# Kernel optimization log

Measured on AMD Instinct MI355X. Metric: run time of the kernel, lower is better.

## Reference

```python
import jax, jax.numpy as jnp
import numpy as np

F, LP, NL, DG = 65536, 8, 8192, 64
D = 32  # path_state_dim == link_state_dim
ITERS = 8
MS = {'flow_traffic': (0.5, 2.0), 'flow_length': (0.5, 2.0), 'flow_loss_packet': (0.1, 5.0),
      'flow_propag_delay': (0.2, 3.0), 'link_capacity': (1.0, 1.0)}


def gru_cell(h, x, w, u, b):
    # Keras GRUCell (reset_after=True); gate order z, r, h
    mx = x @ w + b[0]
    mh = h @ u + b[1]
    xz, xr, xh = jnp.split(mx, 3, axis=-1)
    hz, hr, hh = jnp.split(mh, 3, axis=-1)
    z = jax.nn.sigmoid(xz + hz)
    r = jax.nn.sigmoid(xr + hr)
    c = jnp.tanh(xh + r * hh)
    return z * h + (1.0 - z) * c


def setup_inputs() -> dict:
    key = jax.random.key(0)
    ks = jax.random.split(key, 24)
    g = lambda i, shape: jax.random.normal(ks[i], shape, jnp.float32) * 0.1
    return dict(
        flow_traffic=jax.random.uniform(ks[0], (F, 1), jnp.float32),
        flow_length=jax.random.uniform(ks[1], (F, 1), jnp.float32),
        flow_loss_packet=jax.random.uniform(ks[2], (F, 1), jnp.float32),
        flow_propag_delay=jax.random.uniform(ks[3], (F, 1), jnp.float32),
        flow_packet_size=jax.random.uniform(ks[4], (F, 1), jnp.float32),
        link_capacity=jax.random.uniform(ks[5], (NL, 1), jnp.float32) + 0.5,
        link_to_flow=jax.random.randint(ks[6], (F, LP), 0, NL),
        flow_to_link_flow=jax.random.randint(ks[7], (NL, DG), 0, F),
        flow_to_link_pos=jax.random.randint(ks[8], (NL, DG), 0, LP + 1),
        fe_w1=g(9, (4, D)), fe_b1=jnp.zeros(D), fe_w2=g(10, (D, D)), fe_b2=jnp.zeros(D),
        le_w1=g(11, (2, D)), le_b1=jnp.zeros(D), le_w2=g(12, (D, D)), le_b2=jnp.zeros(D),
        att_w=g(13, (D, D)), att_b=jnp.zeros(D),
        pg_w=g(14, (D, 3 * D)), pg_u=g(15, (D, 3 * D)), pg_b=jnp.zeros((2, 3 * D)),
        lg_w=g(16, (D, 3 * D)), lg_u=g(17, (D, 3 * D)), lg_b=jnp.zeros((2, 3 * D)),
        ro_w1=g(18, (D, D // 2)), ro_b1=jnp.zeros(D // 2),
        ro_w2=g(19, (D // 2, D // 4)), ro_b2=jnp.zeros(D // 4),
        ro_w3=g(20, (D // 4, 1)), ro_b3=jnp.zeros(1),
    )


def reference(flow_traffic, flow_length, flow_loss_packet, flow_propag_delay, flow_packet_size,
              link_capacity, link_to_flow, flow_to_link_flow, flow_to_link_pos,
              fe_w1, fe_b1, fe_w2, fe_b2, le_w1, le_b1, le_w2, le_b2, att_w, att_b,
              pg_w, pg_u, pg_b, lg_w, lg_u, lg_b, ro_w1, ro_b1, ro_w2, ro_b2, ro_w3, ro_b3):
    norm = lambda x, k: (x - MS[k][0]) * MS[k][1]
    # per-link load: mean of traffic of flows crossing it / capacity  -> [NL,1]
    load = jnp.mean(flow_traffic[flow_to_link_flow], axis=1) / link_capacity
    pf = jnp.concatenate([norm(flow_traffic, 'flow_traffic'), norm(flow_length, 'flow_length'),
                          norm(flow_loss_packet, 'flow_loss_packet'),
                          norm(flow_propag_delay, 'flow_propag_delay')], axis=1)
    path_state = jax.nn.selu(jax.nn.selu(pf @ fe_w1 + fe_b1) @ fe_w2 + fe_b2)  # [F,D]
    lf = jnp.concatenate([norm(link_capacity, 'link_capacity'), load], axis=1)
    link_state = jax.nn.selu(jax.nn.selu(lf @ le_w1 + le_b1) @ le_w2 + le_b2)  # [NL,D]

    pss = None
    for _ in range(ITERS):
        link_gather = link_state[link_to_flow]  # [F,LP,D]
        prev = path_state

        def step(h, x):
            h2 = gru_cell(h, x, pg_w, pg_u, pg_b)
            return h2, h2

        path_state, seq = jax.lax.scan(step, prev, jnp.swapaxes(link_gather, 0, 1))
        seq = jnp.swapaxes(seq, 0, 1)  # [F,LP,D]
        pss = jnp.concatenate([prev[:, None, :], seq], axis=1)  # [F,LP+1,D]
        path_gather = pss[flow_to_link_flow, flow_to_link_pos]  # [NL,DG,D]
        attn = jax.nn.leaky_relu(path_gather @ att_w + att_b, negative_slope=0.2)
        score = jax.nn.softmax(attn, axis=-1)  # K.softmax default axis=-1
        agg = jnp.sum(score * path_gather, axis=1)  # [NL,D]
        link_state = gru_cell(link_state, agg, lg_w, lg_u, lg_b)

    h = jax.nn.selu(pss[:, 1:] @ ro_w1 + ro_b1)
    h = jax.nn.selu(h @ ro_w2 + ro_b2)
    occupancy = jax.nn.softplus(h @ ro_w3 + ro_b3)  # [F,LP,1]
    capacity_gather = link_capacity[link_to_flow]  # [F,LP,1]
    delay = jnp.sum(occupancy / capacity_gather, axis=1)  # [F,1]
    return delay + flow_propag_delay
```

## Files before the change

kernel.cpp:

```cpp
#include <hip/hip_runtime.h>
#include <hip/hip_bf16.h>
#include <cstddef>

#define F_    65536
#define LP_   8
#define NL_   8192
#define DG_   64
#define D_    32
#define ITERS_ 8

typedef short bf16x8 __attribute__((ext_vector_type(8)));
typedef float f32x2 __attribute__((ext_vector_type(2)));
typedef float f32x4 __attribute__((ext_vector_type(4)));
typedef float f32x16 __attribute__((ext_vector_type(16)));
typedef unsigned int u32x4 __attribute__((ext_vector_type(4)));

__device__ __forceinline__ float sigmoidf_(float x) { return 1.0f / (1.0f + __expf(-x)); }
__device__ __forceinline__ float tanhf_(float x)    { return 1.0f - 2.0f / (__expf(2.0f * x) + 1.0f); }
__device__ __forceinline__ float seluf_(float x) {
    const float a = 1.6732632423543772f, s = 1.0507009873554805f;
    return x > 0.0f ? s * x : s * a * (__expf(x) - 1.0f);
}
__device__ __forceinline__ float softplusf_(float x) { return x > 20.0f ? x : log1pf(__expf(x)); }

#define REP32(M) M(0)M(1)M(2)M(3)M(4)M(5)M(6)M(7)M(8)M(9)M(10)M(11)M(12)M(13)M(14)M(15) \
                 M(16)M(17)M(18)M(19)M(20)M(21)M(22)M(23)M(24)M(25)M(26)M(27)M(28)M(29)M(30)M(31)

#define BC32(src, i) __int_as_float(__builtin_amdgcn_ds_swizzle(__float_as_int(src), ((i) << 5)))

__device__ __forceinline__ unsigned int cvtpk_bf16(float a, float b) {
    unsigned int r;
    asm("v_cvt_pk_bf16_f32 %0, %1, %2" : "=v"(r) : "v"(a), "v"(b));
    return r;
}
__device__ __forceinline__ float bf_lo(unsigned int u) { return __uint_as_float(u << 16); }
__device__ __forceinline__ float bf_hi(unsigned int u) { return __uint_as_float(u & 0xFFFF0000u); }

__device__ __forceinline__ void mk_frag_w(f32x4 v0, f32x4 v1, u32x4& uh, u32x4& ul) {
    uh.x = cvtpk_bf16(v0.x, v0.y);
    uh.y = cvtpk_bf16(v0.z, v0.w);
    uh.z = cvtpk_bf16(v1.x, v1.y);
    uh.w = cvtpk_bf16(v1.z, v1.w);
    ul.x = cvtpk_bf16(v0.x - bf_lo(uh.x), v0.y - bf_hi(uh.x));
    ul.y = cvtpk_bf16(v0.z - bf_lo(uh.y), v0.w - bf_hi(uh.y));
    ul.z = cvtpk_bf16(v1.x - bf_lo(uh.z), v1.y - bf_hi(uh.z));
    ul.w = cvtpk_bf16(v1.z - bf_lo(uh.w), v1.w - bf_hi(uh.w));
}
__device__ __forceinline__ void mk_frag(f32x4 v0, f32x4 v1, bf16x8& hi, bf16x8& lo) {
    u32x4 uh, ul;
    mk_frag_w(v0, v1, uh, ul);
    hi = __builtin_bit_cast(bf16x8, uh);
    lo = __builtin_bit_cast(bf16x8, ul);
}

__device__ __forceinline__ int mxoff(int g, int d) { return g * 32 + (d & 15) * 2 + (d >> 4); }

__global__ __launch_bounds__(256) void k_init_path(
    const float* __restrict__ tr, const float* __restrict__ len,
    const float* __restrict__ loss, const float* __restrict__ prop,
    const float* __restrict__ fe_w1, const float* __restrict__ fe_b1,
    const float* __restrict__ fe_w2, const float* __restrict__ fe_b2,
    float* __restrict__ h32)
{
    const int j = threadIdx.x & 31;
    const int half = (threadIdx.x >> 5) & 1;
    float w2c[32];
#pragma unroll
    for (int i = 0; i < 32; i++) w2c[i] = fe_w2[i * 32 + j];
    const float w10 = fe_w1[j], w11 = fe_w1[32 + j], w12 = fe_w1[64 + j], w13 = fe_w1[96 + j];
    const float b1 = fe_b1[j], b2 = fe_b2[j];
    const int wave = (blockIdx.x * blockDim.x + threadIdx.x) >> 6;
    const int nw = (gridDim.x * blockDim.x) >> 6;
    for (int fp = wave; fp < F_ / 2; fp += nw) {
        const int f = fp * 2 + half;
        float p0 = (tr[f]   - 0.5f) * 2.0f;
        float p1 = (len[f]  - 0.5f) * 2.0f;
        float p2 = (loss[f] - 0.1f) * 5.0f;
        float p3 = (prop[f] - 0.2f) * 3.0f;
        float h1 = seluf_(fmaf(p0, w10, fmaf(p1, w11, fmaf(p2, w12, fmaf(p3, w13, b1)))));
        float acc = b2;
#define ISTEP(i) { float hv = BC32(h1, i); acc = fmaf(hv, w2c[i], acc); }
        REP32(ISTEP)
#undef ISTEP
        h32[(size_t)f * 32 + j] = seluf_(acc);
    }
}

__global__ __launch_bounds__(256) void k_init_link(
    const float* __restrict__ tr, const float* __restrict__ cap, const int* __restrict__ f2lf,
    const float* __restrict__ le_w1, const float* __restrict__ le_b1,
    const float* __restrict__ le_w2, const float* __restrict__ le_b2,
    float* __restrict__ link_state)
{
    const int lane = threadIdx.x & 63;
    const int j = lane & 31;
    float w2c[32];
#pragma unroll
    for (int i = 0; i < 32; i++) w2c[i] = le_w2[i * 32 + j];
    const float w10 = le_w1[j], w11 = le_w1[32 + j];
    const float b1 = le_b1[j], b2 = le_b2[j];
    const int wave = (blockIdx.x * blockDim.x + threadIdx.x) >> 6;
    const int nw = (gridDim.x * blockDim.x) >> 6;
    for (int l = wave; l < NL_; l += nw) {
        int fidx = f2lf[l * 64 + lane];
        float s = tr[fidx];
        s += __shfl_xor(s, 1);  s += __shfl_xor(s, 2);  s += __shfl_xor(s, 4);
        s += __shfl_xor(s, 8);  s += __shfl_xor(s, 16); s += __shfl_xor(s, 32);
        float c = cap[l];
        float load = s * (1.0f / 64.0f) / c;
        float lf0 = (c - 1.0f);
        float h1 = seluf_(fmaf(lf0, w10, fmaf(load, w11, b1)));
        float acc = b2;
#define LSTEP(i) { float hv = BC32(h1, i); acc = fmaf(hv, w2c[i], acc); }
        REP32(LSTEP)
#undef LSTEP
        if (lane < 32) link_state[l * 32 + j] = seluf_(acc);
    }
}

__global__ __launch_bounds__(256) void k_mx_link(
    const float* __restrict__ link_state, const float* __restrict__ pg_w,
    const float* __restrict__ pg_b, float* __restrict__ mx_link)
{
    const int j = threadIdx.x & 31;
    const int half = (threadIdx.x >> 5) & 1;
    float wz[32], wr[32], wh[32];
#pragma unroll
    for (int i = 0; i < 32; i++) {
        wz[i] = pg_w[i * 96 + j];
        wr[i] = pg_w[i * 96 + 32 + j];
        wh[i] = pg_w[i * 96 + 64 + j];
    }
    const float b0z = pg_b[j], b0r = pg_b[32 + j], b0h = pg_b[64 + j];
    const int wave = (blockIdx.x * blockDim.x + threadIdx.x) >> 6;
    const int nw = (gridDim.x * blockDim.x) >> 6;
    for (int lp = wave; lp < NL_ / 2; lp += nw) {
        const int l = lp * 2 + half;
        float ls = link_state[l * 32 + j];
        float az = b0z, ar = b0r, ah = b0h;
#define MSTEP(i) { float lv = BC32(ls, i); az = fmaf(lv, wz[i], az); ar = fmaf(lv, wr[i], ar); ah = fmaf(lv, wh[i], ah); }
        REP32(MSTEP)
#undef MSTEP
        float* mp = mx_link + l * 96;
        mp[mxoff(0, j)] = az; mp[mxoff(1, j)] = ar; mp[mxoff(2, j)] = ah;
    }
}

__global__ __launch_bounds__(256, 3) void k_path(
    const float* __restrict__ mx_link, const float* __restrict__ pg_u,
    const float* __restrict__ pg_b, const int* __restrict__ l2f,
    unsigned short* __restrict__ pss_bf, float* __restrict__ h32)
{
    __shared__ __align__(16) float xlds[4][576];
    __shared__ u32x4 wfrag[2][6][64];
    const int lane = threadIdx.x & 63;
    const int wid = threadIdx.x >> 6;
    const int jj = lane & 15;
    const int g4 = lane >> 4;
    const int task = (blockIdx.x * blockDim.x + threadIdx.x) >> 6;
    const int fb = task * 16;
    const int frow = fb + 4 * g4;

    for (int tl = wid; tl < 6; tl += 4) {
        const float* up = pg_u + (g4 * 8) * 96 + tl * 16 + jj;
        f32x4 v0 = f32x4{up[0],   up[96],  up[192], up[288]};
        f32x4 v1 = f32x4{up[384], up[480], up[576], up[672]};
        u32x4 uh, ul;
        mk_frag_w(v0, v1, uh, ul);
        wfrag[0][tl][lane] = uh;
        wfrag[1][tl][lane] = ul;
    }
    __syncthreads();

    float b1v[6];
#pragma unroll
    for (int g = 0; g < 3; g++) {
#pragma unroll
        for (int hf = 0; hf < 2; hf++)
            b1v[g * 2 + hf] = pg_b[96 + g * 32 + hf * 16 + jj];
    }
    unsigned short* pbase = pss_bf + (size_t)(fb + jj) * 288;
    float* hbase = h32 + (size_t)(fb + jj) * 32;
    f32x4 v0 = *(const f32x4*)(hbase + g4 * 8);
    f32x4 v1 = *(const f32x4*)(hbase + g4 * 8 + 4);
    bf16x8 ahi, alo;
    {
        u32x4 uh, ul;
        mk_frag_w(v0, v1, uh, ul);
        *(u32x4*)(pbase + g4 * 8) = uh;
        ahi = __builtin_bit_cast(bf16x8, uh);
        alo = __builtin_bit_cast(bf16x8, ul);
    }
    float hC[4][2];
#pragma unroll
    for (int r = 0; r < 4; r++) {
        const float* hp = h32 + (size_t)(fb + 4 * g4 + r) * 32;
        hC[r][0] = hp[jj];
        hC[r][1] = hp[jj + 16];
    }
    float* wl = &xlds[wid][0];

    int lk1[4];
    f32x2 mxn[3][4];
#pragma unroll
    for (int r = 0; r < 4; r++) {
        int lk0 = l2f[(frow + r) * 8 + 0];
        const float* mp = mx_link + lk0 * 96;
#pragma unroll
        for (int g = 0; g < 3; g++)
            mxn[g][r] = *(const f32x2*)(mp + g * 32 + jj * 2);
    }
#pragma unroll
    for (int r = 0; r < 4; r++) lk1[r] = l2f[(frow + r) * 8 + 1];

#pragma unroll
    for (int t = 0; t < 8; t++) {
        f32x2 mxv[3][4];
#pragma unroll
        for (int g = 0; g < 3; g++)
#pragma unroll
            for (int r = 0; r < 4; r++) mxv[g][r] = mxn[g][r];
        if (t < 7) {
#pragma unroll
            for (int r = 0; r < 4; r++) {
                const float* mp = mx_link + lk1[r] * 96;
#pragma unroll
                for (int g = 0; g < 3; g++)
                    mxn[g][r] = *(const f32x2*)(mp + g * 32 + jj * 2);
            }
            if (t < 6) {
#pragma unroll
                for (int r = 0; r < 4; r++)
                    lk1[r] = l2f[(frow + r) * 8 + t + 2];
            }
        }
        f32x4 acc[6];
#pragma unroll
        for (int tl = 0; tl < 6; tl++) {
            int tlx = tl;
            asm volatile("" : "+v"(tlx));
            bf16x8 bh = __builtin_bit_cast(bf16x8, wfrag[0][tlx][lane]);
            bf16x8 bl = __builtin_bit_cast(bf16x8, wfrag[1][tlx][lane]);
            acc[tl] = f32x4{0.0f, 0.0f, 0.0f, 0.0f};
            acc[tl] = __builtin_amdgcn_mfma_f32_16x16x32_bf16(ahi, bh, acc[tl], 0, 0, 0);
            acc[tl] = __builtin_amdgcn_mfma_f32_16x16x32_bf16(ahi, bl, acc[tl], 0, 0, 0);
            acc[tl] = __builtin_amdgcn_mfma_f32_16x16x32_bf16(alo, bh, acc[tl], 0, 0, 0);
        }
#pragma unroll
        for (int r = 0; r < 4; r++) {
#pragma unroll
            for (int hf = 0; hf < 2; hf++) {
                float z  = sigmoidf_(mxv[0][r][hf] + acc[0 + hf][r] + b1v[0 + hf]);
                float rg = sigmoidf_(mxv[1][r][hf] + acc[2 + hf][r] + b1v[2 + hf]);
                float c  = tanhf_(mxv[2][r][hf] + rg * (acc[4 + hf][r] + b1v[4 + hf]));
                float hn = fmaf(z, hC[r][hf], (1.0f - z) * c);
                hC[r][hf] = hn;
                wl[(4 * g4 + r) * 36 + jj + hf * 16] = hn;
            }
        }
        f32x4 n0 = *(const f32x4*)&wl[jj * 36 + g4 * 8];
        f32x4 n1 = *(const f32x4*)&wl[jj * 36 + g4 * 8 + 4];
        u32x4 uh, ul;
        mk_frag_w(n0, n1, uh, ul);
        *(u32x4*)(pbase + (t + 1) * 32 + g4 * 8) = uh;
        if (t < 7) {
            ahi = __builtin_bit_cast(bf16x8, uh);
            alo = __builtin_bit_cast(bf16x8, ul);
        } else {
            *(f32x4*)(hbase + g4 * 8)     = n0;
            *(f32x4*)(hbase + g4 * 8 + 4) = n1;
        }
    }
}

__global__ __launch_bounds__(256, 3) void k_att_fused(
    const unsigned short* __restrict__ pss_bf, const int* __restrict__ f2lf, const int* __restrict__ f2lp,
    const float* __restrict__ att_w, const float* __restrict__ att_b,
    const float* __restrict__ lg_w, const float* __restrict__ lg_u, const float* __restrict__ lg_b,
    const float* __restrict__ pg_w, const float* __restrict__ pg_b,
    float* __restrict__ link_state, float* __restrict__ mx_link)
{
    __shared__ float xbuf[4][32];
    const int w = threadIdx.x >> 6;
    const int lane = threadIdx.x & 63;
    const int p31 = lane & 31;
    const int h = lane >> 5;
    const int l = blockIdx.x * 4 + w;
    const int j = p31;

    const int fi = f2lf[l * 64 + lane];
    const int pi = f2lp[l * 64 + lane];
    const unsigned int* rowp = (const unsigned int*)(pss_bf + ((size_t)fi * 9 + pi) * 32);
    u32x4 g0 = *(const u32x4*)(rowp + 0);
    u32x4 g1 = *(const u32x4*)(rowp + 4);
    u32x4 g2 = *(const u32x4*)(rowp + 8);
    u32x4 g3 = *(const u32x4*)(rowp + 12);
    unsigned int own[16] = {g0.x, g0.y, g0.z, g0.w, g1.x, g1.y, g1.z, g1.w,
                            g2.x, g2.y, g2.z, g2.w, g3.x, g3.y, g3.z, g3.w};
    unsigned int swp[16];
#pragma unroll
    for (int i = 0; i < 16; i++) swp[i] = __shfl_xor(own[i], 32);

    bf16x8 awhi[2], awlo[2];
#pragma unroll
    for (int kt = 0; kt < 2; kt++) {
        const float* wp = att_w + (kt * 16 + h * 8) * 32 + p31;
        f32x4 a0 = f32x4{wp[0],   wp[32],  wp[64],  wp[96]};
        f32x4 a1 = f32x4{wp[128], wp[160], wp[192], wp[224]};
        mk_frag(a0, a1, awhi[kt], awlo[kt]);
    }
    f32x4 ab[4];
#pragma unroll
    for (int rg = 0; rg < 4; rg++) {
        const float* bp = att_b + 8 * rg + 4 * h;
        ab[rg] = f32x4{bp[0], bp[1], bp[2], bp[3]};
    }

    bf16x8 B0[2], B1[2];
#pragma unroll
    for (int kt = 0; kt < 2; kt++) {
        u32x4 b0, b1;
#pragma unroll
        for (int e = 0; e < 4; e++) {
            unsigned int v0 = h ? swp[8 * kt + 4 + e] : own[8 * kt + e];
            unsigned int v1 = h ? own[8 * kt + 4 + e] : swp[8 * kt + e];
            ((unsigned int*)&b0)[e] = v0;
            ((unsigned int*)&b1)[e] = v1;
        }
        B0[kt] = __builtin_bit_cast(bf16x8, b0);
        B1[kt] = __builtin_bit_cast(bf16x8, b1);
    }

    f32x16 acc0{}, acc1{};
#pragma unroll
    for (int kt = 0; kt < 2; kt++) {
        acc0 = __builtin_amdgcn_mfma_f32_32x32x16_bf16(awhi[kt], B0[kt], acc0, 0, 0, 0);
        acc0 = __builtin_amdgcn_mfma_f32_32x32x16_bf16(awlo[kt], B0[kt], acc0, 0, 0, 0);
        acc1 = __builtin_amdgcn_mfma_f32_32x32x16_bf16(awhi[kt], B1[kt], acc1, 0, 0, 0);
        acc1 = __builtin_amdgcn_mfma_f32_32x32x16_bf16(awlo[kt], B1[kt], acc1, 0, 0, 0);
    }

    float q0[16], q1[16];
#pragma unroll
    for (int ph = 0; ph < 2; ph++) {
        float v[16];
#pragma unroll
        for (int r = 0; r < 16; r++) {
            float bias = ((const float*)&ab[r >> 2])[r & 3];
            float x = (ph == 0 ? acc0[r] : acc1[r]) + bias;
            v[r] = x > 0.0f ? x : 0.2f * x;
        }
        float m = v[0];
#pragma unroll
        for (int r = 1; r < 16; r++) m = fmaxf(m, v[r]);
        m = fmaxf(m, __shfl_xor(m, 32));
        float sm = 0.0f;
#pragma unroll
        for (int r = 0; r < 16; r++) { v[r] = __expf(v[r] - m); sm += v[r]; }
        sm += __shfl_xor(sm, 32);
        float inv = 1.0f / sm;
        float* q = (ph == 0) ? q0 : q1;
#pragma unroll
        for (int r = 0; r < 16; r++) {
            const int q4 = r >> 2, s = (r & 3) >> 1;
            unsigned int pv;
            if (ph == 0) pv = h ? swp[4 * q4 + 2 + s] : own[4 * q4 + s];
            else         pv = h ? own[4 * q4 + 2 + s] : swp[4 * q4 + s];
            float pf = (r & 1) ? bf_hi(pv) : bf_lo(pv);
            q[r] = v[r] * inv * pf;
        }
    }
    float qs[16];
#pragma unroll
    for (int r = 0; r < 16; r++) qs[r] = q0[r] + q1[r];
#pragma unroll
    for (int d = 1; d < 32; d <<= 1) {
#pragma unroll
        for (int r = 0; r < 16; r++) qs[r] += __shfl_xor(qs[r], d);
    }
    if (p31 == 0) {
#pragma unroll
        for (int r = 0; r < 16; r++) xbuf[w][(r & 3) + 8 * (r >> 2) + 4 * h] = qs[r];
    }
    float s = xbuf[w][j];

    const float hval = link_state[l * 32 + j];
    float src = (lane < 32) ? hval : s;
    const float* wb = (lane < 32) ? lg_u : lg_w;
    float p0 = (lane < 32) ? lg_b[96 + j]      : lg_b[j];
    float p1 = (lane < 32) ? lg_b[96 + 32 + j] : lg_b[32 + j];
    float p2 = (lane < 32) ? lg_b[96 + 64 + j] : lg_b[64 + j];
#define ASTEP(i) { float vv = BC32(src, i); \
    p0 = fmaf(vv, wb[(i) * 96 + j], p0); \
    p1 = fmaf(vv, wb[(i) * 96 + 32 + j], p1); \
    p2 = fmaf(vv, wb[(i) * 96 + 64 + j], p2); }
    REP32(ASTEP)
#undef ASTEP
    float t0 = __shfl_xor(p0, 32);
    float t1 = __shfl_xor(p1, 32);
    float t2 = __shfl_xor(p2, 32);
    float hn = 0.0f;
    if (lane < 32) {
        float z = sigmoidf_(t0 + p0);
        float r = sigmoidf_(t1 + p1);
        float c = tanhf_(t2 + r * p2);
        hn = fmaf(z, hval, (1.0f - z) * c);
        link_state[l * 32 + j] = hn;
    }
    float hnb = __shfl(hn, j);
    float m0 = (lane < 32) ? pg_b[j]      : pg_b[64 + j];
    float m1 = (lane < 32) ? pg_b[32 + j] : 0.0f;
    const float* c0 = (lane < 32) ? pg_w + j      : pg_w + 64 + j;
    const float* c1 = (lane < 32) ? pg_w + 32 + j : pg_w + 64 + j;
#define MXS(i) { float vv = BC32(hnb, i); \
    m0 = fmaf(vv, c0[(i) * 96], m0); \
    m1 = fmaf(vv, c1[(i) * 96], m1); }
    REP32(MXS)
#undef MXS
    float* mp = mx_link + l * 96;
    if (lane < 32) { mp[mxoff(0, j)] = m0; mp[mxoff(1, j)] = m1; }
    else           { mp[mxoff(2, j)] = m0; }
}

__global__ __launch_bounds__(256) void k_readout(
    const unsigned short* __restrict__ pss_bf, const int* __restrict__ l2f,
    const float* __restrict__ cap, const float* __restrict__ prop,
    const float* __restrict__ ro_w1, const float* __restrict__ b1,
    const float* __restrict__ ro_w2, const float* __restrict__ b2,
    const float* __restrict__ w3, const float* __restrict__ b3,
    float* __restrict__ out)
{
    const int tid = blockIdx.x * blockDim.x + threadIdx.x;
    const int f = tid >> 3, t = tid & 7;
    const unsigned int* rowp = (const unsigned int*)(pss_bf + ((size_t)f * 9 + 1 + t) * 32);
    float xr[32];
#pragma unroll
    for (int i = 0; i < 4; i++) {
        u32x4 v = *(const u32x4*)(rowp + 4 * i);
        xr[8 * i + 0] = bf_lo(v.x); xr[8 * i + 1] = bf_hi(v.x);
        xr[8 * i + 2] = bf_lo(v.y); xr[8 * i + 3] = bf_hi(v.y);
        xr[8 * i + 4] = bf_lo(v.z); xr[8 * i + 5] = bf_hi(v.z);
        xr[8 * i + 6] = bf_lo(v.w); xr[8 * i + 7] = bf_hi(v.w);
    }
    float h1[16];
#pragma unroll
    for (int jj = 0; jj < 16; jj++) {
        float acc = b1[jj];
#pragma unroll
        for (int i = 0; i < 32; i++) acc = fmaf(xr[i], ro_w1[i * 16 + jj], acc);
        h1[jj] = seluf_(acc);
    }
    float h2[8];
#pragma unroll
    for (int jj = 0; jj < 8; jj++) {
        float acc = b2[jj];
#pragma unroll
        for (int i = 0; i < 16; i++) acc = fmaf(h1[i], ro_w2[i * 8 + jj], acc);
        h2[jj] = seluf_(acc);
    }
    float o = b3[0];
#pragma unroll
    for (int i = 0; i < 8; i++) o = fmaf(h2[i], w3[i], o);
    o = softplusf_(o);
    int link = l2f[f * 8 + t];
    float v = o / cap[link];
    v += __shfl_xor(v, 1, 8);
    v += __shfl_xor(v, 2, 8);
    v += __shfl_xor(v, 4, 8);
    if (t == 0) out[f] = v + prop[f];
}

extern "C" void kernel_launch(void* const* d_in, const int* in_sizes, int n_in,
                              void* d_out, int out_size, void* d_ws, size_t ws_size,
                              hipStream_t stream) {
    const float* flow_traffic = (const float*)d_in[0];
    const float* flow_length  = (const float*)d_in[1];
    const float* flow_loss    = (const float*)d_in[2];
    const float* flow_prop    = (const float*)d_in[3];
    const float* link_cap     = (const float*)d_in[5];
    const int*   l2f          = (const int*)d_in[6];
    const int*   f2lf         = (const int*)d_in[7];
    const int*   f2lp         = (const int*)d_in[8];
    const float* fe_w1 = (const float*)d_in[9],  *fe_b1 = (const float*)d_in[10];
    const float* fe_w2 = (const float*)d_in[11], *fe_b2 = (const float*)d_in[12];
    const float* le_w1 = (const float*)d_in[13], *le_b1 = (const float*)d_in[14];
    const float* le_w2 = (const float*)d_in[15], *le_b2 = (const float*)d_in[16];
    const float* att_w = (const float*)d_in[17], *att_b = (const float*)d_in[18];
    const float* pg_w  = (const float*)d_in[19], *pg_u  = (const float*)d_in[20], *pg_b = (const float*)d_in[21];
    const float* lg_w  = (const float*)d_in[22], *lg_u  = (const float*)d_in[23], *lg_b = (const float*)d_in[24];
    const float* ro_w1 = (const float*)d_in[25], *ro_b1 = (const float*)d_in[26];
    const float* ro_w2 = (const float*)d_in[27], *ro_b2 = (const float*)d_in[28];
    const float* ro_w3 = (const float*)d_in[29], *ro_b3 = (const float*)d_in[30];
    float* out = (float*)d_out;

    unsigned short* pss_bf = (unsigned short*)d_ws;
    float* h32        = (float*)(pss_bf + (size_t)F_ * 288);
    float* link_state = h32 + (size_t)F_ * 32;
    float* mx_link    = link_state + NL_ * 32;

    k_init_path<<<512, 256, 0, stream>>>(flow_traffic, flow_length, flow_loss, flow_prop,
                                         fe_w1, fe_b1, fe_w2, fe_b2, h32);
    k_init_link<<<512, 256, 0, stream>>>(flow_traffic, link_cap, f2lf,
                                         le_w1, le_b1, le_w2, le_b2, link_state);
    k_mx_link<<<64, 256, 0, stream>>>(link_state, pg_w, pg_b, mx_link);
    for (int it = 0; it < ITERS_; ++it) {
        k_path<<<F_ / 64, 256, 0, stream>>>(mx_link, pg_u, pg_b, l2f, pss_bf, h32);
        k_att_fused<<<NL_ / 4, 256, 0, stream>>>(pss_bf, f2lf, f2lp, att_w, att_b,
                                                 lg_w, lg_u, lg_b, pg_w, pg_b,
                                                 link_state, mx_link);
    }
    k_readout<<<F_ * 8 / 256, 256, 0, stream>>>(pss_bf, l2f, link_cap, flow_prop,
                                                ro_w1, ro_b1, ro_w2, ro_b2, ro_w3, ro_b3, out);
}
```

Measured before the change: 585.3 us.

## Compute path GRU input projection in-kernel via MFMA from packed bf16 link state

Drops the precomputed per-link input projection (mx_link, 96 floats per link) and instead stores link state as split hi/lo bf16 pairs (ls_pack). The path GRU kernel now gathers this compact 32-dim state and does x@W with extra MFMAs alongside h@U, with biases folded together. This removes the k_mx_link launch and the per-link projection in the attention kernel, and cuts the gather size per step. The cost is more matrix-core work and LDS for weight fragments in the path kernel, which may raise register pressure.

```diff
diff --git a/kernel.cpp b/kernel.cpp
--- a/kernel.cpp
+++ b/kernel.cpp
@@ -52,8 +52,6 @@
     hi = __builtin_bit_cast(bf16x8, uh);
     lo = __builtin_bit_cast(bf16x8, ul);
 }
-
-__device__ __forceinline__ int mxoff(int g, int d) { return g * 32 + (d & 15) * 2 + (d >> 4); }
 
 __global__ __launch_bounds__(256) void k_init_path(
     const float* __restrict__ tr, const float* __restrict__ len,
@@ -90,7 +88,7 @@
     const float* __restrict__ tr, const float* __restrict__ cap, const int* __restrict__ f2lf,
     const float* __restrict__ le_w1, const float* __restrict__ le_b1,
     const float* __restrict__ le_w2, const float* __restrict__ le_b2,
-    float* __restrict__ link_state)
+    float* __restrict__ link_state, unsigned int* __restrict__ ls_pack)
 {
     const int lane = threadIdx.x & 63;
     const int j = lane & 31;
@@ -114,55 +112,37 @@
 #define LSTEP(i) { float hv = BC32(h1, i); acc = fmaf(hv, w2c[i], acc); }
         REP32(LSTEP)
 #undef LSTEP
-        if (lane < 32) link_state[l * 32 + j] = seluf_(acc);
-    }
-}
-
-__global__ __launch_bounds__(256) void k_mx_link(
-    const float* __restrict__ link_state, const float* __restrict__ pg_w,
-    const float* __restrict__ pg_b, float* __restrict__ mx_link)
-{
-    const int j = threadIdx.x & 31;
-    const int half = (threadIdx.x >> 5) & 1;
-    float wz[32], wr[32], wh[32];
-#pragma unroll
-    for (int i = 0; i < 32; i++) {
-        wz[i] = pg_w[i * 96 + j];
-        wr[i] = pg_w[i * 96 + 32 + j];
-        wh[i] = pg_w[i * 96 + 64 + j];
-    }
-    const float b0z = pg_b[j], b0r = pg_b[32 + j], b0h = pg_b[64 + j];
-    const int wave = (blockIdx.x * blockDim.x + threadIdx.x) >> 6;
-    const int nw = (gridDim.x * blockDim.x) >> 6;
-    for (int lp = wave; lp < NL_ / 2; lp += nw) {
-        const int l = lp * 2 + half;
-        float ls = link_state[l * 32 + j];
-        float az = b0z, ar = b0r, ah = b0h;
-#define MSTEP(i) { float lv = BC32(ls, i); az = fmaf(lv, wz[i], az); ar = fmaf(lv, wr[i], ar); ah = fmaf(lv, wh[i], ah); }
-        REP32(MSTEP)
-#undef MSTEP
-        float* mp = mx_link + l * 96;
-        mp[mxoff(0, j)] = az; mp[mxoff(1, j)] = ar; mp[mxoff(2, j)] = ah;
+        float lsv = seluf_(acc);
+        float a = __shfl(lsv, 2 * (j & 15));
+        float b = __shfl(lsv, 2 * (j & 15) + 1);
+        unsigned int hw = cvtpk_bf16(a, b);
+        unsigned int lw = cvtpk_bf16(a - bf_lo(hw), b - bf_hi(hw));
+        if (lane < 32) {
+            link_state[l * 32 + j] = lsv;
+            ls_pack[l * 32 + j] = (j < 16) ? hw : lw;
+        }
     }
 }
 
 __global__ __launch_bounds__(256, 3) void k_path(
-    const float* __restrict__ mx_link, const float* __restrict__ pg_u,
-    const float* __restrict__ pg_b, const int* __restrict__ l2f,
+    const unsigned int* __restrict__ ls_pack, const float* __restrict__ pg_u,
+    const float* __restrict__ pg_w, const float* __restrict__ pg_b,
+    const int* __restrict__ l2f,
     unsigned short* __restrict__ pss_bf, float* __restrict__ h32)
 {
     __shared__ __align__(16) float xlds[4][576];
-    __shared__ u32x4 wfrag[2][6][64];
+    __shared__ u32x4 wfrag[2][12][64];
     const int lane = threadIdx.x & 63;
     const int wid = threadIdx.x >> 6;
     const int jj = lane & 15;
     const int g4 = lane >> 4;
     const int task = (blockIdx.x * blockDim.x + threadIdx.x) >> 6;
     const int fb = task * 16;
-    const int frow = fb + 4 * g4;
-
-    for (int tl = wid; tl < 6; tl += 4) {
-        const float* up = pg_u + (g4 * 8) * 96 + tl * 16 + jj;
+
+    for (int tl = wid; tl < 12; tl += 4) {
+        const float* base = (tl < 6) ? pg_u : pg_w;
+        const int tc = (tl < 6) ? tl : tl - 6;
+        const float* up = base + (g4 * 8) * 96 + tc * 16 + jj;
         f32x4 v0 = f32x4{up[0],   up[96],  up[192], up[288]};
         f32x4 v1 = f32x4{up[384], up[480], up[576], up[672]};
         u32x4 uh, ul;
@@ -172,12 +152,14 @@
     }
     __syncthreads();
 
-    float b1v[6];
-#pragma unroll
-    for (int g = 0; g < 3; g++) {
-#pragma unroll
-        for (int hf = 0; hf < 2; hf++)
-            b1v[g * 2 + hf] = pg_b[96 + g * 32 + hf * 16 + jj];
+    float b_z[2], b_r[2], b_0h[2], b_1h[2];
+#pragma unroll
+    for (int hf = 0; hf < 2; hf++) {
+        const int idx = hf * 16 + jj;
+        b_z[hf]  = pg_b[idx]      + pg_b[96 + idx];
+        b_r[hf]  = pg_b[32 + idx] + pg_b[96 + 32 + idx];
+        b_0h[hf] = pg_b[64 + idx];
+        b_1h[hf] = pg_b[96 + 64 + idx];
     }
     unsigned short* pbase = pss_bf + (size_t)(fb + jj) * 288;
     float* hbase = h32 + (size_t)(fb + jj) * 32;
@@ -200,60 +182,57 @@
     }
     float* wl = &xlds[wid][0];
 
-    int lk1[4];
-    f32x2 mxn[3][4];
-#pragma unroll
-    for (int r = 0; r < 4; r++) {
-        int lk0 = l2f[(frow + r) * 8 + 0];
-        const float* mp = mx_link + lk0 * 96;
-#pragma unroll
-        for (int g = 0; g < 3; g++)
-            mxn[g][r] = *(const f32x2*)(mp + g * 32 + jj * 2);
-    }
-#pragma unroll
-    for (int r = 0; r < 4; r++) lk1[r] = l2f[(frow + r) * 8 + 1];
+    int lks[8];
+    {
+        const int* lrow = l2f + (fb + jj) * 8;
+#pragma unroll
+        for (int t = 0; t < 8; t++) lks[t] = lrow[t];
+    }
+    const u32x4* lsp = (const u32x4*)ls_pack;
+    u32x4 lsh_n = lsp[lks[0] * 8 + g4];
+    u32x4 lsl_n = lsp[lks[0] * 8 + 4 + g4];
 
 #pragma unroll
     for (int t = 0; t < 8; t++) {
-        f32x2 mxv[3][4];
-#pragma unroll
-        for (int g = 0; g < 3; g++)
-#pragma unroll
-            for (int r = 0; r < 4; r++) mxv[g][r] = mxn[g][r];
+        bf16x8 xhi = __builtin_bit_cast(bf16x8, lsh_n);
+        bf16x8 xlo = __builtin_bit_cast(bf16x8, lsl_n);
         if (t < 7) {
-#pragma unroll
-            for (int r = 0; r < 4; r++) {
-                const float* mp = mx_link + lk1[r] * 96;
-#pragma unroll
-                for (int g = 0; g < 3; g++)
-                    mxn[g][r] = *(const f32x2*)(mp + g * 32 + jj * 2);
-            }
-            if (t < 6) {
-#pragma unroll
-                for (int r = 0; r < 4; r++)
-                    lk1[r] = l2f[(frow + r) * 8 + t + 2];
-            }
-        }
-        f32x4 acc[6];
+            lsh_n = lsp[lks[t + 1] * 8 + g4];
+            lsl_n = lsp[lks[t + 1] * 8 + 4 + g4];
+        }
+        f32x4 acc[8];
+#pragma unroll
+        for (int a = 0; a < 8; a++) acc[a] = f32x4{0.0f, 0.0f, 0.0f, 0.0f};
 #pragma unroll
         for (int tl = 0; tl < 6; tl++) {
             int tlx = tl;
             asm volatile("" : "+v"(tlx));
             bf16x8 bh = __builtin_bit_cast(bf16x8, wfrag[0][tlx][lane]);
             bf16x8 bl = __builtin_bit_cast(bf16x8, wfrag[1][tlx][lane]);
-            acc[tl] = f32x4{0.0f, 0.0f, 0.0f, 0.0f};
-            acc[tl] = __builtin_amdgcn_mfma_f32_16x16x32_bf16(ahi, bh, acc[tl], 0, 0, 0);
-            acc[tl] = __builtin_amdgcn_mfma_f32_16x16x32_bf16(ahi, bl, acc[tl], 0, 0, 0);
-            acc[tl] = __builtin_amdgcn_mfma_f32_16x16x32_bf16(alo, bh, acc[tl], 0, 0, 0);
+            const int a = (tl < 4) ? tl : 4 + (tl & 1);
+            acc[a] = __builtin_amdgcn_mfma_f32_16x16x32_bf16(ahi, bh, acc[a], 0, 0, 0);
+            acc[a] = __builtin_amdgcn_mfma_f32_16x16x32_bf16(ahi, bl, acc[a], 0, 0, 0);
+            acc[a] = __builtin_amdgcn_mfma_f32_16x16x32_bf16(alo, bh, acc[a], 0, 0, 0);
+        }
+#pragma unroll
+        for (int tl = 0; tl < 6; tl++) {
+            int tlx = 6 + tl;
+            asm volatile("" : "+v"(tlx));
+            bf16x8 bh = __builtin_bit_cast(bf16x8, wfrag[0][tlx][lane]);
+            bf16x8 bl = __builtin_bit_cast(bf16x8, wfrag[1][tlx][lane]);
+            const int a = (tl < 4) ? tl : 6 + (tl & 1);
+            acc[a] = __builtin_amdgcn_mfma_f32_16x16x32_bf16(xhi, bh, acc[a], 0, 0, 0);
+            acc[a] = __builtin_amdgcn_mfma_f32_16x16x32_bf16(xhi, bl, acc[a], 0, 0, 0);
+            acc[a] = __builtin_amdgcn_mfma_f32_16x16x32_bf16(xlo, bh, acc[a], 0, 0, 0);
         }
 #pragma unroll
         for (int r = 0; r < 4; r++) {
 #pragma unroll
             for (int hf = 0; hf < 2; hf++) {
-                float z  = sigmoidf_(mxv[0][r][hf] + acc[0 + hf][r] + b1v[0 + hf]);
-                float rg = sigmoidf_(mxv[1][r][hf] + acc[2 + hf][r] + b1v[2 + hf]);
-                float c  = tanhf_(mxv[2][r][hf] + rg * (acc[4 + hf][r] + b1v[4 + hf]));
-                float hn = fmaf(z, hC[r][hf], (1.0f - z) * c);
+                float z  = sigmoidf_(acc[0 + hf][r] + b_z[hf]);
+                float rg = sigmoidf_(acc[2 + hf][r] + b_r[hf]);
+                float c  = tanhf_(acc[6 + hf][r] + b_0h[hf] + rg * (acc[4 + hf][r] + b_1h[hf]));
+                float hn = fmaf(z, hC[r][hf] - c, c);
                 hC[r][hf] = hn;
                 wl[(4 * g4 + r) * 36 + jj + hf * 16] = hn;
             }
@@ -277,8 +256,7 @@
     const unsigned short* __restrict__ pss_bf, const int* __restrict__ f2lf, const int* __restrict__ f2lp,
     const float* __restrict__ att_w, const float* __restrict__ att_b,
     const float* __restrict__ lg_w, const float* __restrict__ lg_u, const float* __restrict__ lg_b,
-    const float* __restrict__ pg_w, const float* __restrict__ pg_b,
-    float* __restrict__ link_state, float* __restrict__ mx_link)
+    float* __restrict__ link_state, unsigned int* __restrict__ ls_pack)
 {
     __shared__ float xbuf[4][32];
     const int w = threadIdx.x >> 6;
@@ -407,19 +385,11 @@
         hn = fmaf(z, hval, (1.0f - z) * c);
         link_state[l * 32 + j] = hn;
     }
-    float hnb = __shfl(hn, j);
-    float m0 = (lane < 32) ? pg_b[j]      : pg_b[64 + j];
-    float m1 = (lane < 32) ? pg_b[32 + j] : 0.0f;
-    const float* c0 = (lane < 32) ? pg_w + j      : pg_w + 64 + j;
-    const float* c1 = (lane < 32) ? pg_w + 32 + j : pg_w + 64 + j;
-#define MXS(i) { float vv = BC32(hnb, i); \
-    m0 = fmaf(vv, c0[(i) * 96], m0); \
-    m1 = fmaf(vv, c1[(i) * 96], m1); }
-    REP32(MXS)
-#undef MXS
-    float* mp = mx_link + l * 96;
-    if (lane < 32) { mp[mxoff(0, j)] = m0; mp[mxoff(1, j)] = m1; }
-    else           { mp[mxoff(2, j)] = m0; }
+    float a = __shfl(hn, 2 * (j & 15));
+    float b = __shfl(hn, 2 * (j & 15) + 1);
+    unsigned int hw = cvtpk_bf16(a, b);
+    unsigned int lw = cvtpk_bf16(a - bf_lo(hw), b - bf_hi(hw));
+    if (lane < 32) ls_pack[l * 32 + j] = (j < 16) ? hw : lw;
 }
 
 __global__ __launch_bounds__(256) void k_readout(
@@ -496,18 +466,16 @@
     unsigned short* pss_bf = (unsigned short*)d_ws;
     float* h32        = (float*)(pss_bf + (size_t)F_ * 288);
     float* link_state = h32 + (size_t)F_ * 32;
-    float* mx_link    = link_state + NL_ * 32;
+    unsigned int* ls_pack = (unsigned int*)(link_state + NL_ * 32);
 
     k_init_path<<<512, 256, 0, stream>>>(flow_traffic, flow_length, flow_loss, flow_prop,
                                          fe_w1, fe_b1, fe_w2, fe_b2, h32);
     k_init_link<<<512, 256, 0, stream>>>(flow_traffic, link_cap, f2lf,
-                                         le_w1, le_b1, le_w2, le_b2, link_state);
-    k_mx_link<<<64, 256, 0, stream>>>(link_state, pg_w, pg_b, mx_link);
+                                         le_w1, le_b1, le_w2, le_b2, link_state, ls_pack);
     for (int it = 0; it < ITERS_; ++it) {
-        k_path<<<F_ / 64, 256, 0, stream>>>(mx_link, pg_u, pg_b, l2f, pss_bf, h32);
+        k_path<<<F_ / 64, 256, 0, stream>>>(ls_pack, pg_u, pg_w, pg_b, l2f, pss_bf, h32);
         k_att_fused<<<NL_ / 4, 256, 0, stream>>>(pss_bf, f2lf, f2lp, att_w, att_b,
-                                                 lg_w, lg_u, lg_b, pg_w, pg_b,
-                                                 link_state, mx_link);
+                                                 lg_w, lg_u, lg_b, link_state, ls_pack);
     }
     k_readout<<<F_ * 8 / 256, 256, 0, stream>>>(pss_bf, l2f, link_cap, flow_prop,
                                                 ro_w1, ro_b1, ro_w2, ro_b2, ro_w3, ro_b3, out);
```

Result: faster. 560.3 us (-4.3%).
